# Optimization experiments

Measured on AMD Instinct MI355X. Metric: run time of the kernel, lower is better.

Reference implementation:

```python
import jax, jax.numpy as jnp
import numpy as np

B, IN_DIM, OUT_DIM = 4096, 4096, 4096

def setup_inputs() -> dict:
    key = jax.random.key(0)
    kx, kw, kb = jax.random.split(key, 3)
    x = jax.random.normal(kx, (B, IN_DIM), dtype=jnp.float32)
    W = jax.random.normal(kw, (OUT_DIM, IN_DIM), dtype=jnp.float32) * (1.0 / np.sqrt(IN_DIM))
    b = jax.random.normal(kb, (OUT_DIM,), dtype=jnp.float32) * (1.0 / np.sqrt(IN_DIM))
    return {"x": x, "W": W, "b": b}

def reference(x, W, b):
    # Original computes sum over in_dim of x[:, :, None] * W.T[None, :, :],
    # which is exactly x @ W.T. NOTE: bias is added TWICE in the source
    # (duplicated `out += self.b`), so the faithful output is x @ W.T + 2*b.
    out = jnp.einsum('bi,oi->bo', x, W)  # [B, out_dim]
    out = out + 2.0 * b
    return out
```

## Files before the change

kernel.cpp:

```cpp
#include <hip/hip_runtime.h>
#include <hip/hip_bf16.h>
#include <utility>


typedef short bf16x8 __attribute__((ext_vector_type(8)));
typedef short s16x4  __attribute__((ext_vector_type(4)));
typedef short s16x8  __attribute__((ext_vector_type(8)));
typedef float f32x4  __attribute__((ext_vector_type(4)));

constexpr int MDIM = 4096, NDIM = 4096, KDIM = 4096;

typedef const __attribute__((address_space(1))) void* gas_t;
typedef __attribute__((address_space(3))) void*       las_t;

__device__ __forceinline__ short f2bf(float f) {
    __hip_bfloat16 h = __float2bfloat16(f);
    short s; __builtin_memcpy(&s, &h, 2); return s;
}

__global__ __launch_bounds__(256)
void cvt2_f32_bf16(const float* __restrict__ inA, const float* __restrict__ inB,
                   short* __restrict__ outA, short* __restrict__ outB, int n8each) {
    int idx    = blockIdx.x * blockDim.x + threadIdx.x;
    int stride = gridDim.x * blockDim.x;
    for (int i = idx; i < 2 * n8each; i += stride) {
        const f32x4* in4 = (i < n8each) ? (const f32x4*)inA : (const f32x4*)inB;
        s16x8*      out8 = (i < n8each) ? (s16x8*)outA      : (s16x8*)outB;
        int j = (i < n8each) ? i : i - n8each;
        f32x4 a = in4[2 * j];
        f32x4 b = in4[2 * j + 1];
        s16x8 o = { f2bf(a[0]), f2bf(a[1]), f2bf(a[2]), f2bf(a[3]),
                    f2bf(b[0]), f2bf(b[1]), f2bf(b[2]), f2bf(b[3]) };
        out8[j] = o;
    }
}

constexpr int BM = 256, BN = 256, BK = 64;
constexpr int NT  = KDIM / BK;
constexpr int ASZ = BM * BK;
constexpr int BSZ = BN * BK;

template <int Q>
__device__ __forceinline__ void read_aq(const short* base, int rA, int c0, int c1,
                                        bf16x8 (&dst)[2][2]) {
    #pragma unroll
    for (int m = 0; m < 2; ++m) {
        const short* p = &base[(rA + Q * 32 + m * 16) * BK];
        dst[m][0] = *(const bf16x8*)(p + c0);
        dst[m][1] = *(const bf16x8*)(p + c1);
    }
}

template <int Q>
__device__ __forceinline__ void mfma_quad(const bf16x8 (&af)[2][2], const bf16x8 (&bf)[4][2],
                                          f32x4 (&acc)[8][4]) {
    __builtin_amdgcn_s_setprio(1);
    #pragma unroll
    for (int m = 0; m < 2; ++m)
        #pragma unroll
        for (int ni = 0; ni < 4; ++ni)
            #pragma unroll
            for (int kk = 0; kk < 2; ++kk)
                acc[Q * 2 + m][ni] = __builtin_amdgcn_mfma_f32_16x16x32_bf16(
                    af[m][kk], bf[ni][kk], acc[Q * 2 + m][ni], 0, 0, 0);
    __builtin_amdgcn_s_setprio(0);
}

__global__ __launch_bounds__(512, 2)
void gemm_bf16_256(const short* __restrict__ Xb, const short* __restrict__ Wb,
                   const float* __restrict__ Bv, float* __restrict__ Out)
{
    __shared__ short lds[2 * ASZ + 2 * BSZ];

    const int tid  = threadIdx.x;
    const int lane = tid & 63;
    const int wid  = tid >> 6;
    const int wr   = wid >> 2;
    const int wc   = wid & 3;

    const int bid = blockIdx.x;
    const int lin = (bid & 7) * 32 + (bid >> 3);
    const int tm0 = (lin >> 4) * BM;
    const int tn0 = (lin & 15) * BN;

    const int srow = lane >> 3;
    const int sgrn = (lane & 7) ^ srow;
    const char* xbase = (const char*)Xb;
    const char* wbase = (const char*)Wb;
    int aOff[2][2], bOff[2][2], dOff[2][2];
    #pragma unroll
    for (int h = 0; h < 2; ++h) {
        #pragma unroll
        for (int j = 0; j < 2; ++j) {
            const int r = h * 128 + (2 * wid + j) * 8;
            aOff[h][j] = ((tm0 + r + srow) * KDIM + sgrn * 8) * 2;
            bOff[h][j] = ((tn0 + r + srow) * KDIM + sgrn * 8) * 2;
            dOff[h][j] = r * BK;
        }
    }

    const int g   = lane >> 4;
    const int r16 = lane & 15;
    const int c0  = ((0 + g) ^ (r16 & 7)) * 8;
    const int c1  = ((4 + g) ^ (r16 & 7)) * 8;
    const int rA  = wr * 128 + r16;
    const int rB  = wc * 64  + r16;

    f32x4 acc[8][4] = {};
    bf16x8 bf[4][2];
    bf16x8 a0[2][2];

    auto tile_body = [&](auto par_ic, int t) {
        constexpr int PAR = decltype(par_ic)::value;
        const short* Ab  = (const short*)&lds[PAR * ASZ];
        const short* AbN = (const short*)&lds[(PAR ^ 1) * ASZ];
        const short* BbN = (const short*)&lds[2 * ASZ + (PAR ^ 1) * BSZ];
        short* dstA = (short*)&lds[(PAR ^ 1) * ASZ];
        short* dstB = (short*)&lds[2 * ASZ + PAR * BSZ];

        auto stageA = [&](int kt, int h) {
            const size_t kb = (size_t)kt * (BK * 2);
            __builtin_amdgcn_global_load_lds((gas_t)(xbase + kb + aOff[h][0]),
                                             (las_t)(dstA + dOff[h][0]), 16, 0, 0);
            __builtin_amdgcn_global_load_lds((gas_t)(xbase + kb + aOff[h][1]),
                                             (las_t)(dstA + dOff[h][1]), 16, 0, 0);
        };
        auto stageB = [&](int kt, int h) {
            const size_t kb = (size_t)kt * (BK * 2);
            __builtin_amdgcn_global_load_lds((gas_t)(wbase + kb + bOff[h][0]),
                                             (las_t)(dstB + dOff[h][0]), 16, 0, 0);
            __builtin_amdgcn_global_load_lds((gas_t)(wbase + kb + bOff[h][1]),
                                             (las_t)(dstB + dOff[h][1]), 16, 0, 0);
        };

        bf16x8 aq1[2][2];
        read_aq<1>(Ab, rA, c0, c1, aq1);
        if (t + 1 < NT) { stageA(t + 1, 0); stageA(t + 1, 1); }
        mfma_quad<0>(a0, bf, acc);

        bf16x8 aq2[2][2];
        read_aq<2>(Ab, rA, c0, c1, aq2);
        if (t + 2 < NT) stageB(t + 2, 0);
        mfma_quad<1>(aq1, bf, acc);

        bf16x8 aq3[2][2];
        read_aq<3>(Ab, rA, c0, c1, aq3);
        if (t + 2 < NT) stageB(t + 2, 1);
        mfma_quad<2>(aq2, bf, acc);
        if (t < NT - 2) { asm volatile("s_waitcnt vmcnt(4)" ::: "memory"); }
        else            { asm volatile("s_waitcnt vmcnt(0)" ::: "memory"); }
        asm volatile("s_barrier" ::: "memory");

        __builtin_amdgcn_s_setprio(1);
        #pragma unroll
        for (int ni = 0; ni < 4; ++ni) {
            #pragma unroll
            for (int kk = 0; kk < 2; ++kk) {
                const int cc = kk ? c1 : c0;
                acc[6][ni] = __builtin_amdgcn_mfma_f32_16x16x32_bf16(
                                 aq3[0][kk], bf[ni][kk], acc[6][ni], 0, 0, 0);
                acc[7][ni] = __builtin_amdgcn_mfma_f32_16x16x32_bf16(
                                 aq3[1][kk], bf[ni][kk], acc[7][ni], 0, 0, 0);
                if (t + 1 < NT)
                    bf[ni][kk] = *(const bf16x8*)(&BbN[(rB + ni * 16) * BK] + cc);
            }
        }
        __builtin_amdgcn_s_setprio(0);
        if (t + 1 < NT) read_aq<0>(AbN, rA, c0, c1, a0);
        asm volatile("s_barrier" ::: "memory");
    };

    {
        short* dA0 = (short*)&lds[0];
        short* dB0 = (short*)&lds[2 * ASZ];
        short* dB1 = (short*)&lds[2 * ASZ + BSZ];
        #pragma unroll
        for (int h = 0; h < 2; ++h) {
            __builtin_amdgcn_global_load_lds((gas_t)(wbase + bOff[h][0]), (las_t)(dB0 + dOff[h][0]), 16, 0, 0);
            __builtin_amdgcn_global_load_lds((gas_t)(wbase + bOff[h][1]), (las_t)(dB0 + dOff[h][1]), 16, 0, 0);
        }
        #pragma unroll
        for (int h = 0; h < 2; ++h) {
            __builtin_amdgcn_global_load_lds((gas_t)(xbase + aOff[h][0]), (las_t)(dA0 + dOff[h][0]), 16, 0, 0);
            __builtin_amdgcn_global_load_lds((gas_t)(xbase + aOff[h][1]), (las_t)(dA0 + dOff[h][1]), 16, 0, 0);
        }
        #pragma unroll
        for (int h = 0; h < 2; ++h) {
            __builtin_amdgcn_global_load_lds((gas_t)(wbase + (BK * 2) + bOff[h][0]), (las_t)(dB1 + dOff[h][0]), 16, 0, 0);
            __builtin_amdgcn_global_load_lds((gas_t)(wbase + (BK * 2) + bOff[h][1]), (las_t)(dB1 + dOff[h][1]), 16, 0, 0);
        }
        asm volatile("s_waitcnt vmcnt(4)" ::: "memory");
        asm volatile("s_barrier" ::: "memory");
        const short* Bb0 = (const short*)&lds[2 * ASZ];
        #pragma unroll
        for (int ni = 0; ni < 4; ++ni) {
            const short* p = &Bb0[(rB + ni * 16) * BK];
            bf[ni][0] = *(const bf16x8*)(p + c0);
            bf[ni][1] = *(const bf16x8*)(p + c1);
        }
        read_aq<0>((const short*)&lds[0], rA, c0, c1, a0);
    }

    for (int t = 0; t < NT; t += 2) {
        tile_body(std::integral_constant<int, 0>{}, t);
        tile_body(std::integral_constant<int, 1>{}, t + 1);
    }

    float bb[4];
    #pragma unroll
    for (int ni = 0; ni < 4; ++ni)
        bb[ni] = 2.0f * Bv[tn0 + wc * 64 + ni * 16 + r16];

    #pragma unroll
    for (int mi = 0; mi < 8; ++mi) {
        #pragma unroll
        for (int r = 0; r < 4; ++r) {
            const int row = tm0 + wr * 128 + mi * 16 + g * 4 + r;
            float* orow = Out + (size_t)row * NDIM + tn0 + wc * 64 + r16;
            #pragma unroll
            for (int ni = 0; ni < 4; ++ni)
                orow[ni * 16] = acc[mi][ni][r] + bb[ni];
        }
    }
}

constexpr int FBM = 128, FBN = 128, FBK = 32, LDT = FBK + 8;
__global__ __launch_bounds__(256)
void gemm_xwt_bias2(const float* __restrict__ X, const float* __restrict__ W,
                    const float* __restrict__ Bv, float* __restrict__ Out)
{
    __shared__ short As[FBM * LDT];
    __shared__ short Bs[FBN * LDT];
    const int tid  = threadIdx.x;
    const int lane = tid & 63;
    const int wid  = tid >> 6;
    const int wr   = wid >> 1;
    const int wc   = wid & 1;
    const int tm0  = blockIdx.y * FBM;
    const int tn0  = blockIdx.x * FBN;
    const int srow = tid >> 3;
    const int scol = (tid & 7) * 4;
    const int g    = lane >> 4;
    const int r16  = lane & 15;
    f32x4 acc[4][4] = {};
    const float* xg = X + (size_t)(tm0 + srow) * KDIM + scol;
    const float* wg = W + (size_t)(tn0 + srow) * KDIM + scol;
    for (int k0 = 0; k0 < KDIM; k0 += FBK) {
        #pragma unroll
        for (int i = 0; i < 4; ++i) {
            const int row = srow + 32 * i;
            f32x4 av = *(const f32x4*)(xg + (size_t)(32 * i) * KDIM + k0);
            f32x4 bv = *(const f32x4*)(wg + (size_t)(32 * i) * KDIM + k0);
            s16x4 pa = { f2bf(av[0]), f2bf(av[1]), f2bf(av[2]), f2bf(av[3]) };
            s16x4 pb = { f2bf(bv[0]), f2bf(bv[1]), f2bf(bv[2]), f2bf(bv[3]) };
            *(s16x4*)&As[row * LDT + scol] = pa;
            *(s16x4*)&Bs[row * LDT + scol] = pb;
        }
        __syncthreads();
        bf16x8 af[4], bfr[4];
        #pragma unroll
        for (int mi = 0; mi < 4; ++mi)
            af[mi] = *(const bf16x8*)&As[(wr * 64 + mi * 16 + r16) * LDT + g * 8];
        #pragma unroll
        for (int ni = 0; ni < 4; ++ni)
            bfr[ni] = *(const bf16x8*)&Bs[(wc * 64 + ni * 16 + r16) * LDT + g * 8];
        #pragma unroll
        for (int mi = 0; mi < 4; ++mi)
            #pragma unroll
            for (int ni = 0; ni < 4; ++ni)
                acc[mi][ni] = __builtin_amdgcn_mfma_f32_16x16x32_bf16(
                                  af[mi], bfr[ni], acc[mi][ni], 0, 0, 0);
        __syncthreads();
    }
    float bb[4];
    #pragma unroll
    for (int ni = 0; ni < 4; ++ni)
        bb[ni] = 2.0f * Bv[tn0 + wc * 64 + ni * 16 + r16];
    #pragma unroll
    for (int mi = 0; mi < 4; ++mi)
        #pragma unroll
        for (int r = 0; r < 4; ++r) {
            const int row = tm0 + wr * 64 + mi * 16 + g * 4 + r;
            float* orow = Out + (size_t)row * NDIM + tn0 + wc * 64 + r16;
            #pragma unroll
            for (int ni = 0; ni < 4; ++ni)
                orow[ni * 16] = acc[mi][ni][r] + bb[ni];
        }
}

extern "C" void kernel_launch(void* const* d_in, const int* in_sizes, int n_in,
                              void* d_out, int out_size, void* d_ws, size_t ws_size,
                              hipStream_t stream) {
    const float* X  = (const float*)d_in[0];
    const float* W  = (const float*)d_in[1];
    const float* Bv = (const float*)d_in[2];
    float* Out = (float*)d_out;

    const size_t nElem = (size_t)MDIM * KDIM;
    const size_t need  = 2 * nElem * sizeof(short);

    if (ws_size >= need) {
        short* Xb = (short*)d_ws;
        short* Wb = Xb + nElem;
        const int n8 = (int)(nElem / 8);
        cvt2_f32_bf16<<<4096, 256, 0, stream>>>(X, W, Xb, Wb, n8);
        gemm_bf16_256<<<dim3(256), 512, 0, stream>>>(Xb, Wb, Bv, Out);
    } else {
        dim3 grid(NDIM / FBN, MDIM / FBM);
        gemm_xwt_bias2<<<grid, 256, 0, stream>>>(X, W, Bv, Out);
    }
}
```

Measured before the change: 145.7 us.

## Triple-buffer A tiles in LDS to prefetch two k-tiles ahead

Adds a third LDS slot for the A operand so A tiles are staged two iterations ahead like B, with rotating buffer pointers replacing the parity-templated loop body. The wait count is relaxed to allow more outstanding loads, and the barrier is moved before the third MFMA group. This aims to hide global-load latency better, at the cost of more LDS per block (possibly reducing occupancy) and runtime pointer rotation instead of compile-time addresses.

New measurement: 135.5 us (median of 2 runs). 7.0% less time.

```diff
diff --git a/kernel.cpp b/kernel.cpp
--- a/kernel.cpp
+++ b/kernel.cpp
@@ -1,6 +1,5 @@
 #include <hip/hip_runtime.h>
 #include <hip/hip_bf16.h>
-#include <utility>
 
 
 typedef short bf16x8 __attribute__((ext_vector_type(8)));
@@ -70,7 +69,7 @@
 void gemm_bf16_256(const short* __restrict__ Xb, const short* __restrict__ Wb,
                    const float* __restrict__ Bv, float* __restrict__ Out)
 {
-    __shared__ short lds[2 * ASZ + 2 * BSZ];
+    __shared__ short lds[3 * ASZ + 2 * BSZ];
 
     const int tid  = threadIdx.x;
     const int lane = tid & 63;
@@ -110,46 +109,68 @@
     bf16x8 bf[4][2];
     bf16x8 a0[2][2];
 
-    auto tile_body = [&](auto par_ic, int t) {
-        constexpr int PAR = decltype(par_ic)::value;
-        const short* Ab  = (const short*)&lds[PAR * ASZ];
-        const short* AbN = (const short*)&lds[(PAR ^ 1) * ASZ];
-        const short* BbN = (const short*)&lds[2 * ASZ + (PAR ^ 1) * BSZ];
-        short* dstA = (short*)&lds[(PAR ^ 1) * ASZ];
-        short* dstB = (short*)&lds[2 * ASZ + PAR * BSZ];
-
-        auto stageA = [&](int kt, int h) {
-            const size_t kb = (size_t)kt * (BK * 2);
-            __builtin_amdgcn_global_load_lds((gas_t)(xbase + kb + aOff[h][0]),
-                                             (las_t)(dstA + dOff[h][0]), 16, 0, 0);
-            __builtin_amdgcn_global_load_lds((gas_t)(xbase + kb + aOff[h][1]),
-                                             (las_t)(dstA + dOff[h][1]), 16, 0, 0);
-        };
-        auto stageB = [&](int kt, int h) {
-            const size_t kb = (size_t)kt * (BK * 2);
-            __builtin_amdgcn_global_load_lds((gas_t)(wbase + kb + bOff[h][0]),
-                                             (las_t)(dstB + dOff[h][0]), 16, 0, 0);
-            __builtin_amdgcn_global_load_lds((gas_t)(wbase + kb + bOff[h][1]),
-                                             (las_t)(dstB + dOff[h][1]), 16, 0, 0);
-        };
-
+    auto stageA = [&](int kt, int h, short* dst) {
+        const size_t kb = (size_t)kt * (BK * 2);
+        __builtin_amdgcn_global_load_lds((gas_t)(xbase + kb + aOff[h][0]),
+                                         (las_t)(dst + dOff[h][0]), 16, 0, 0);
+        __builtin_amdgcn_global_load_lds((gas_t)(xbase + kb + aOff[h][1]),
+                                         (las_t)(dst + dOff[h][1]), 16, 0, 0);
+    };
+    auto stageB = [&](int kt, int h, short* dst) {
+        const size_t kb = (size_t)kt * (BK * 2);
+        __builtin_amdgcn_global_load_lds((gas_t)(wbase + kb + bOff[h][0]),
+                                         (las_t)(dst + dOff[h][0]), 16, 0, 0);
+        __builtin_amdgcn_global_load_lds((gas_t)(wbase + kb + bOff[h][1]),
+                                         (las_t)(dst + dOff[h][1]), 16, 0, 0);
+    };
+
+    short* aSlot0 = (short*)&lds[0];
+    short* aSlot1 = (short*)&lds[ASZ];
+    short* aSlot2 = (short*)&lds[2 * ASZ];
+    short* bSlot0 = (short*)&lds[3 * ASZ];
+    short* bSlot1 = (short*)&lds[3 * ASZ + BSZ];
+
+    {
+        #pragma unroll
+        for (int h = 0; h < 2; ++h) stageB(0, h, bSlot0);
+        #pragma unroll
+        for (int h = 0; h < 2; ++h) stageA(0, h, aSlot0);
+        #pragma unroll
+        for (int h = 0; h < 2; ++h) stageB(1, h, bSlot1);
+        #pragma unroll
+        for (int h = 0; h < 2; ++h) stageA(1, h, aSlot1);
+        asm volatile("s_waitcnt vmcnt(8)" ::: "memory");
+        asm volatile("s_barrier" ::: "memory");
+        #pragma unroll
+        for (int ni = 0; ni < 4; ++ni) {
+            const short* p = &bSlot0[(rB + ni * 16) * BK];
+            bf[ni][0] = *(const bf16x8*)(p + c0);
+            bf[ni][1] = *(const bf16x8*)(p + c1);
+        }
+        read_aq<0>(aSlot0, rA, c0, c1, a0);
+    }
+
+    short* aCur = aSlot0; short* aNxt = aSlot1; short* aStg = aSlot2;
+    short* bCur = bSlot0; short* bNxt = bSlot1;
+
+    for (int t = 0; t < NT; ++t) {
         bf16x8 aq1[2][2];
-        read_aq<1>(Ab, rA, c0, c1, aq1);
-        if (t + 1 < NT) { stageA(t + 1, 0); stageA(t + 1, 1); }
+        read_aq<1>(aCur, rA, c0, c1, aq1);
+        if (t + 2 < NT) { stageA(t + 2, 0, aStg); stageA(t + 2, 1, aStg); }
         mfma_quad<0>(a0, bf, acc);
 
         bf16x8 aq2[2][2];
-        read_aq<2>(Ab, rA, c0, c1, aq2);
-        if (t + 2 < NT) stageB(t + 2, 0);
+        read_aq<2>(aCur, rA, c0, c1, aq2);
+        if (t + 2 < NT) stageB(t + 2, 0, bCur);
         mfma_quad<1>(aq1, bf, acc);
 
         bf16x8 aq3[2][2];
-        read_aq<3>(Ab, rA, c0, c1, aq3);
-        if (t + 2 < NT) stageB(t + 2, 1);
-        mfma_quad<2>(aq2, bf, acc);
-        if (t < NT - 2) { asm volatile("s_waitcnt vmcnt(4)" ::: "memory"); }
+        read_aq<3>(aCur, rA, c0, c1, aq3);
+        if (t + 2 < NT) stageB(t + 2, 1, bCur);
+        if (t < NT - 2) { asm volatile("s_waitcnt vmcnt(8)" ::: "memory"); }
         else            { asm volatile("s_waitcnt vmcnt(0)" ::: "memory"); }
         asm volatile("s_barrier" ::: "memory");
+        mfma_quad<2>(aq2, bf, acc);
 
         __builtin_amdgcn_s_setprio(1);
         #pragma unroll
@@ -162,48 +183,15 @@
                 acc[7][ni] = __builtin_amdgcn_mfma_f32_16x16x32_bf16(
                                  aq3[1][kk], bf[ni][kk], acc[7][ni], 0, 0, 0);
                 if (t + 1 < NT)
-                    bf[ni][kk] = *(const bf16x8*)(&BbN[(rB + ni * 16) * BK] + cc);
+                    bf[ni][kk] = *(const bf16x8*)(&bNxt[(rB + ni * 16) * BK] + cc);
             }
         }
         __builtin_amdgcn_s_setprio(0);
-        if (t + 1 < NT) read_aq<0>(AbN, rA, c0, c1, a0);
+        if (t + 1 < NT) read_aq<0>(aNxt, rA, c0, c1, a0);
         asm volatile("s_barrier" ::: "memory");
-    };
-
-    {
-        short* dA0 = (short*)&lds[0];
-        short* dB0 = (short*)&lds[2 * ASZ];
-        short* dB1 = (short*)&lds[2 * ASZ + BSZ];
-        #pragma unroll
-        for (int h = 0; h < 2; ++h) {
-            __builtin_amdgcn_global_load_lds((gas_t)(wbase + bOff[h][0]), (las_t)(dB0 + dOff[h][0]), 16, 0, 0);
-            __builtin_amdgcn_global_load_lds((gas_t)(wbase + bOff[h][1]), (las_t)(dB0 + dOff[h][1]), 16, 0, 0);
-        }
-        #pragma unroll
-        for (int h = 0; h < 2; ++h) {
-            __builtin_amdgcn_global_load_lds((gas_t)(xbase + aOff[h][0]), (las_t)(dA0 + dOff[h][0]), 16, 0, 0);
-            __builtin_amdgcn_global_load_lds((gas_t)(xbase + aOff[h][1]), (las_t)(dA0 + dOff[h][1]), 16, 0, 0);
-        }
-        #pragma unroll
-        for (int h = 0; h < 2; ++h) {
-            __builtin_amdgcn_global_load_lds((gas_t)(wbase + (BK * 2) + bOff[h][0]), (las_t)(dB1 + dOff[h][0]), 16, 0, 0);
-            __builtin_amdgcn_global_load_lds((gas_t)(wbase + (BK * 2) + bOff[h][1]), (las_t)(dB1 + dOff[h][1]), 16, 0, 0);
-        }
-        asm volatile("s_waitcnt vmcnt(4)" ::: "memory");
-        asm volatile("s_barrier" ::: "memory");
-        const short* Bb0 = (const short*)&lds[2 * ASZ];
-        #pragma unroll
-        for (int ni = 0; ni < 4; ++ni) {
-            const short* p = &Bb0[(rB + ni * 16) * BK];
-            bf[ni][0] = *(const bf16x8*)(p + c0);
-            bf[ni][1] = *(const bf16x8*)(p + c1);
-        }
-        read_aq<0>((const short*)&lds[0], rA, c0, c1, a0);
-    }
-
-    for (int t = 0; t < NT; t += 2) {
-        tile_body(std::integral_constant<int, 0>{}, t);
-        tile_body(std::integral_constant<int, 1>{}, t + 1);
+
+        short* tmp = aCur; aCur = aNxt; aNxt = aStg; aStg = tmp;
+        tmp = bCur; bCur = bNxt; bNxt = tmp;
     }
 
     float bb[4];
```
